# Optimization experiments

Measured on AMD Instinct MI355X. Metric: run time of the kernel, lower is better.

## Reference

```python
import jax, jax.numpy as jnp
import numpy as np

# Hardcoded non-tensor forward args (kernels_desc / kernels_radius / input dims):
# kernels_desc = [{'weight': 1.0, 'xy': 6.0, 'image': 0.1}], kernels_radius = [3, 3, 3]
# height_input = width_input = depth_input = prediction resolution (pool is identity).
R0, R1 = 3, 3
WEIGHT = 1.0
SIGMA_XY = 6.0
SIGMA_IMG = 0.1


def _unfold(img, r0, r1):
    # torch unfoldNd equivalent: (N, C, kh, kw, H*W), zero padding, stride 1.
    N, C, H, W = img.shape
    p = jnp.pad(img, ((0, 0), (0, 0), (r0, r0), (r1, r1)))
    shifts = [p[:, :, i:i + H, j:j + W]
              for i in range(2 * r0 + 1) for j in range(2 * r1 + 1)]
    out = jnp.stack(shifts, axis=2)  # (N, C, kh*kw, H, W)
    return out.reshape(N, C, 2 * r0 + 1, 2 * r1 + 1, H * W)


def _forward(y_hat_softmax, sample):
    N, C, H, W, D = y_hat_softmax.shape
    Ci = sample.shape[1]
    NB = N * D
    # fold depth into batch: (N*D, C, H, W)
    y = y_hat_softmax.transpose(0, 4, 1, 2, 3).reshape(NB, C, H, W)
    s = sample.transpose(0, 4, 1, 2, 3).reshape(NB, Ci, H, W)
    # adaptive_avg_pool2d to (H, W): input res == pred res here -> identity.
    # xy mesh features (row index channel, then col index channel)
    rows = jnp.broadcast_to(jnp.arange(H, dtype=y.dtype)[None, None, :, None], (NB, 1, H, W))
    cols = jnp.broadcast_to(jnp.arange(W, dtype=y.dtype)[None, None, None, :], (NB, 1, H, W))
    feats = jnp.concatenate([rows / SIGMA_XY, cols / SIGMA_XY, s / SIGMA_IMG], axis=1)
    # Gaussian affinity kernel over local windows
    fu = _unfold(feats, R0, R1)                         # (NB, Cf, kh, kw, HW)
    center = fu[:, :, R0, R1, :][:, :, None, None, :]
    k = WEIGHT * jnp.exp(-0.5 * ((fu - center) ** 2).sum(axis=1, keepdims=True))
    k = k.at[:, :, R0, R1, :].set(0.0)                  # zero self-affinity
    # weighted sum of neighbor predictions
    yu = _unfold(y, R0, R1)                             # (NB, C, kh, kw, HW)
    kh_kw = (2 * R0 + 1) * (2 * R1 + 1)
    prod = (k * yu).reshape(NB, C, kh_kw, H * W).sum(axis=2).reshape(NB, C, H, W)
    loss = k.sum() - (prod * y).sum()
    denom = NB * H * W
    return loss / denom


def setup_inputs() -> dict:
    key = jax.random.key(0)
    k1, k2 = jax.random.split(key)
    N, C, H, W, D = 2, 2, 64, 64, 64
    logits = jax.random.normal(k1, (N, C, H, W, D), dtype=jnp.float32)
    y = jax.nn.softmax(logits, axis=1)  # prediction must be a softmax over channels
    sample = jax.random.normal(k2, (N, 1, H, W, D), dtype=jnp.float32)
    return {"y_hat_softmax": y, "sample": sample}


def reference(y_hat_softmax, sample):
    return _forward(y_hat_softmax, sample)
```

## Files before the change

kernel.cpp:

```cpp
#include <hip/hip_runtime.h>


constexpr int N = 2, H = 64, W = 64, D = 64, R = 3;
constexpr int WD  = W * D;
constexpr int HWD = H * W * D;
constexpr float INV_SXY  = 1.0f / 6.0f;
constexpr float INV_SIMG = 10.0f;
constexpr int NBLOCKS = N * H * (W / 16);

__global__ __launch_bounds__(256) void crf_partial(
    const float* __restrict__ y,
    const float* __restrict__ s,
    float* __restrict__ partial) {
    const int tid   = threadIdx.x;
    const int d0    = (tid & 15) << 2;
    const int wlane = tid >> 4;
    const int bid   = blockIdx.x;
    const int w = ((bid & 3) << 4) + wlane;
    const int h = (bid >> 2) & 63;
    const int n = bid >> 8;

    const float* sb  = s + (size_t)n * HWD;
    const float* y0b = y + (size_t)n * (2 * HWD);

    const int cidx = h * WD + w * D + d0;
    const float4 sc4 = *(const float4*)(sb  + cidx);
    const float4 b4  = *(const float4*)(y0b + cidx);
    const float scv[4] = {sc4.x, sc4.y, sc4.z, sc4.w};
    const float bv[4]  = {b4.x,  b4.y,  b4.z,  b4.w};

    float acc[4] = {0.f, 0.f, 0.f, 0.f};

    #pragma unroll
    for (int di = 0; di <= R; ++di) {
        const int hh = h + di;
        const bool rowok = hh < H;
        #pragma unroll
        for (int dj = (di == 0 ? 1 : -R); dj <= R; ++dj) {
            const int ww = w + dj;
            if (rowok && (unsigned)ww < (unsigned)W) {
                const int idx = hh * WD + ww * D + d0;
                const float4 sn4 = *(const float4*)(sb  + idx);
                const float4 a4  = *(const float4*)(y0b + idx);
                const float A = -0.5f * (float)(di * di + dj * dj) *
                                (INV_SXY * INV_SXY);
                const float snv[4] = {sn4.x, sn4.y, sn4.z, sn4.w};
                const float av[4]  = {a4.x,  a4.y,  a4.z,  a4.w};
                #pragma unroll
                for (int j = 0; j < 4; ++j) {
                    const float dsr = snv[j] - scv[j];
                    const float k = __expf(A - 0.5f * (INV_SIMG * INV_SIMG) *
                                                   dsr * dsr);
                    const float t = av[j] + bv[j] - 2.0f * av[j] * bv[j];
                    acc[j] += k * t;
                }
            }
        }
    }

    float part = 2.0f * (acc[0] + acc[1] + acc[2] + acc[3]);

    const int nrows = min(h + R, H - 1) - max(h - R, 0) + 1;
    const int ncols = min(w + R, W - 1) - max(w - R, 0) + 1;
    const int oob = 49 - nrows * ncols;
    if (oob) {
        const float fh = (float)h * INV_SXY;
        const float fw = (float)w * INV_SXY;
        const float base = fh * fh + fw * fw;
        float koob = 0.0f;
        #pragma unroll
        for (int j = 0; j < 4; ++j) {
            const float fs = scv[j] * INV_SIMG;
            koob += __expf(-0.5f * (base + fs * fs));
        }
        part += (float)oob * koob;
    }

    #pragma unroll
    for (int off = 32; off; off >>= 1)
        part += __shfl_down(part, off, 64);

    __shared__ float wsum[4];
    if ((tid & 63) == 0) wsum[tid >> 6] = part;
    __syncthreads();
    if (tid == 0) partial[bid] = wsum[0] + wsum[1] + wsum[2] + wsum[3];
}

__global__ __launch_bounds__(256) void reduce_partials(
    const float* __restrict__ partial, float* __restrict__ out) {
    const int tid = threadIdx.x;
    float v = partial[tid] + partial[tid + 256];
    #pragma unroll
    for (int off = 32; off; off >>= 1)
        v += __shfl_down(v, off, 64);
    __shared__ float wsum[4];
    if ((tid & 63) == 0) wsum[tid >> 6] = v;
    __syncthreads();
    if (tid == 0)
        out[0] = (wsum[0] + wsum[1] + wsum[2] + wsum[3]) *
                 (1.0f / (float)(N * D * H * W));
}

extern "C" void kernel_launch(void* const* d_in, const int* in_sizes, int n_in,
                              void* d_out, int out_size, void* d_ws, size_t ws_size,
                              hipStream_t stream) {
    const float* y = (const float*)d_in[0];
    const float* s = (const float*)d_in[1];
    float* partial = (float*)d_ws;

    crf_partial<<<dim3(NBLOCKS), dim3(256), 0, stream>>>(y, s, partial);
    reduce_partials<<<dim3(1), dim3(256), 0, stream>>>(partial, (float*)d_out);
}
```

Baseline: 65.26 us.

## Split neighbor offsets across two block groups and use native exp2

The grid is doubled: each pixel column is now handled by two blocks, and each block processes half of the 24 forward neighbor offsets (12 each). The out-of-bounds correction is computed only by group 0. The exponential is rewritten as a hardware exp2 with log2e folded into the constants, which removes a multiply per exp. The goal is more parallelism to hide latency in a memory/latency-bound kernel of only 512 blocks. The cost is that center values are loaded twice and the reduction kernel has twice as many partials to sum.

```diff
diff --git a/kernel.cpp b/kernel.cpp
--- a/kernel.cpp
+++ b/kernel.cpp
@@ -5,8 +5,14 @@
 constexpr int WD  = W * D;
 constexpr int HWD = H * W * D;
 constexpr float INV_SXY  = 1.0f / 6.0f;
-constexpr float INV_SIMG = 10.0f;
-constexpr int NBLOCKS = N * H * (W / 16);
+constexpr float LOG2E    = 1.4426950408889634f;
+constexpr float C2       = 50.0f * LOG2E;
+constexpr int GBLOCKS = N * H * (W / 16);
+constexpr int NBLOCKS = 2 * GBLOCKS;
+
+__device__ __forceinline__ float exp2_fast(float x) {
+    return __builtin_amdgcn_exp2f(x);
+}
 
 __global__ __launch_bounds__(256) void crf_partial(
     const float* __restrict__ y,
@@ -16,9 +22,11 @@
     const int d0    = (tid & 15) << 2;
     const int wlane = tid >> 4;
     const int bid   = blockIdx.x;
-    const int w = ((bid & 3) << 4) + wlane;
-    const int h = (bid >> 2) & 63;
-    const int n = bid >> 8;
+    const int sbid  = bid & (GBLOCKS - 1);
+    const int g     = bid >> 9;
+    const int w = ((sbid & 3) << 4) + wlane;
+    const int h = (sbid >> 2) & 63;
+    const int n = sbid >> 8;
 
     const float* sb  = s + (size_t)n * HWD;
     const float* y0b = y + (size_t)n * (2 * HWD);
@@ -31,50 +39,54 @@
 
     float acc[4] = {0.f, 0.f, 0.f, 0.f};
 
-    #pragma unroll
-    for (int di = 0; di <= R; ++di) {
-        const int hh = h + di;
-        const bool rowok = hh < H;
-        #pragma unroll
-        for (int dj = (di == 0 ? 1 : -R); dj <= R; ++dj) {
-            const int ww = w + dj;
-            if (rowok && (unsigned)ww < (unsigned)W) {
-                const int idx = hh * WD + ww * D + d0;
-                const float4 sn4 = *(const float4*)(sb  + idx);
-                const float4 a4  = *(const float4*)(y0b + idx);
-                const float A = -0.5f * (float)(di * di + dj * dj) *
-                                (INV_SXY * INV_SXY);
-                const float snv[4] = {sn4.x, sn4.y, sn4.z, sn4.w};
-                const float av[4]  = {a4.x,  a4.y,  a4.z,  a4.w};
-                #pragma unroll
-                for (int j = 0; j < 4; ++j) {
-                    const float dsr = snv[j] - scv[j];
-                    const float k = __expf(A - 0.5f * (INV_SIMG * INV_SIMG) *
-                                                   dsr * dsr);
-                    const float t = av[j] + bv[j] - 2.0f * av[j] * bv[j];
-                    acc[j] += k * t;
-                }
-            }
-        }
+    #define PAIR(di, dj)                                                      \
+    {                                                                         \
+        const int hh = h + (di);                                              \
+        const int ww = w + (dj);                                              \
+        if (hh < H && (unsigned)ww < (unsigned)W) {                           \
+            const int idx = hh * WD + ww * D + d0;                            \
+            const float4 sn4 = *(const float4*)(sb  + idx);                   \
+            const float4 a4  = *(const float4*)(y0b + idx);                   \
+            const float A2 = -0.5f * (float)((di)*(di) + (dj)*(dj)) *         \
+                             (INV_SXY * INV_SXY) * LOG2E;                     \
+            const float snv[4] = {sn4.x, sn4.y, sn4.z, sn4.w};                \
+            const float av[4]  = {a4.x,  a4.y,  a4.z,  a4.w};                 \
+            _Pragma("unroll")                                                 \
+            for (int j = 0; j < 4; ++j) {                                     \
+                const float dsr = snv[j] - scv[j];                            \
+                const float k = exp2_fast(A2 - C2 * dsr * dsr);               \
+                acc[j] += k * (av[j] + bv[j] - 2.0f * av[j] * bv[j]);         \
+            }                                                                 \
+        }                                                                     \
     }
 
-    float part = 2.0f * (acc[0] + acc[1] + acc[2] + acc[3]);
+    float extra = 0.0f;
+    if (g == 0) {
+        PAIR(0, 1) PAIR(0, 2) PAIR(0, 3)
+        PAIR(1, -3) PAIR(1, -2) PAIR(1, -1) PAIR(1, 0)
+        PAIR(1, 1) PAIR(1, 2) PAIR(1, 3)
+        PAIR(2, -3) PAIR(2, -2)
+        const int nrows = min(h + R, H - 1) - max(h - R, 0) + 1;
+        const int ncols = min(w + R, W - 1) - max(w - R, 0) + 1;
+        const int oob = 49 - nrows * ncols;
+        if (oob) {
+            const float fh = (float)h * INV_SXY;
+            const float fw = (float)w * INV_SXY;
+            const float base2 = -0.5f * (fh * fh + fw * fw) * LOG2E;
+            float koob = 0.0f;
+            #pragma unroll
+            for (int j = 0; j < 4; ++j)
+                koob += exp2_fast(base2 - C2 * scv[j] * scv[j]);
+            extra = (float)oob * koob;
+        }
+    } else {
+        PAIR(2, -1) PAIR(2, 0) PAIR(2, 1) PAIR(2, 2) PAIR(2, 3)
+        PAIR(3, -3) PAIR(3, -2) PAIR(3, -1) PAIR(3, 0)
+        PAIR(3, 1) PAIR(3, 2) PAIR(3, 3)
+    }
+    #undef PAIR
 
-    const int nrows = min(h + R, H - 1) - max(h - R, 0) + 1;
-    const int ncols = min(w + R, W - 1) - max(w - R, 0) + 1;
-    const int oob = 49 - nrows * ncols;
-    if (oob) {
-        const float fh = (float)h * INV_SXY;
-        const float fw = (float)w * INV_SXY;
-        const float base = fh * fh + fw * fw;
-        float koob = 0.0f;
-        #pragma unroll
-        for (int j = 0; j < 4; ++j) {
-            const float fs = scv[j] * INV_SIMG;
-            koob += __expf(-0.5f * (base + fs * fs));
-        }
-        part += (float)oob * koob;
-    }
+    float part = 2.0f * (acc[0] + acc[1] + acc[2] + acc[3]) + extra;
 
     #pragma unroll
     for (int off = 32; off; off >>= 1)
@@ -89,7 +101,10 @@
 __global__ __launch_bounds__(256) void reduce_partials(
     const float* __restrict__ partial, float* __restrict__ out) {
     const int tid = threadIdx.x;
-    float v = partial[tid] + partial[tid + 256];
+    float v = 0.0f;
+    #pragma unroll
+    for (int i = 0; i < NBLOCKS / 256; ++i)
+        v += partial[tid + i * 256];
     #pragma unroll
     for (int off = 32; off; off >>= 1)
         v += __shfl_down(v, off, 64);
```

Result: no change. 64.07 us (-1.8%).
